# Optimization experiments

Measured on AMD Instinct MI355X. Metric: run time of the kernel, lower is better.

Reference implementation:

```python
import jax, jax.numpy as jnp
import numpy as np
from jax import lax

B, S, I, H, O, T = 8, 1024, 512, 1024, 512, 8
THRESH = 0.5


def setup_inputs() -> dict:
    key = jax.random.key(0)
    k = jax.random.split(key, 5)
    return {
        "x": jax.random.normal(k[0], (B, S, I), dtype=jnp.float32),
        "w1": jax.random.normal(k[1], (H, I), dtype=jnp.float32) * (1.0 / np.sqrt(I)),
        "b1": jax.random.normal(k[2], (H,), dtype=jnp.float32) * 0.01,
        "w2": jax.random.normal(k[3], (O, H), dtype=jnp.float32) * (1.0 / np.sqrt(H)),
        "b2": jax.random.normal(k[4], (O,), dtype=jnp.float32) * 0.01,
    }


def reference(x, w1, b1, w2, b2):
    # x: (B, S, I). Precompute the input current once (same every timestep).
    inp_cur = jnp.einsum("bsi,hi->bsh", x, w1) + b1  # (B, S, H)
    mem1_0 = jnp.zeros((B, S, H), dtype=x.dtype)
    mem2_0 = jnp.zeros((B, S, O), dtype=x.dtype)

    def step(carry, _):
        mem1, mem2 = carry
        mem1 = mem1 + inp_cur
        spike1 = (mem1 > THRESH).astype(x.dtype)
        mem1 = mem1 * (mem1 <= THRESH).astype(x.dtype)  # reset fired neurons
        mem2 = mem2 + jnp.einsum("bsh,oh->bso", spike1, w2) + b2
        spike2 = (mem2 > THRESH).astype(x.dtype)
        mem2 = mem2 * (mem2 <= THRESH).astype(x.dtype)
        return (mem1, mem2), spike2

    _, spikes = lax.scan(step, (mem1_0, mem2_0), None, length=T)  # (T, B, S, O)
    return jnp.moveaxis(spikes, 0, 1)  # stack on dim=1 -> (B, T, S, O)
```

## Files before the change

### kernel.cpp

```cpp
#include <hip/hip_runtime.h>

static constexpr int B_ = 8, S_ = 1024, I_ = 512, H_ = 1024, O_ = 512, T_ = 8;
static constexpr int M_ = B_ * S_;
static constexpr float TH = 0.5f;

__global__ __launch_bounds__(256) void k1(const float* __restrict__ X,
                                          const float* __restrict__ W1,
                                          const float* __restrict__ B1,
                                          unsigned char* __restrict__ SPB) {
  __shared__ float As[16][132];
  __shared__ float Bs[16][68];
  const int tid = threadIdx.x;
  const int tx = tid & 15, ty = tid >> 4;
  const int rowBase = blockIdx.x * 128, colBase = blockIdx.y * 64;
  const int rrA = tid >> 2, kqA = (tid & 3) << 2;
  const int rrB = tid >> 2, kqB = (tid & 3) << 2;

  float acc[8][4];
#pragma unroll
  for (int i = 0; i < 8; ++i)
#pragma unroll
    for (int j = 0; j < 4; ++j) acc[i][j] = 0.f;

  float4 pa0, pa1, pb;
#define K1_LOAD(IT)                                                            \
  {                                                                            \
    pa0 = *(const float4*)&X[(size_t)(rowBase + rrA) * I_ + (IT) * 16 + kqA];  \
    pa1 = *(const float4*)&X[(size_t)(rowBase + 64 + rrA) * I_ + (IT) * 16 + kqA]; \
    pb  = *(const float4*)&W1[(size_t)(colBase + rrB) * I_ + (IT) * 16 + kqB]; \
  }

  K1_LOAD(0);
  for (int it = 0; it < 32; ++it) {
    As[kqA + 0][rrA] = pa0.x; As[kqA + 1][rrA] = pa0.y;
    As[kqA + 2][rrA] = pa0.z; As[kqA + 3][rrA] = pa0.w;
    As[kqA + 0][64 + rrA] = pa1.x; As[kqA + 1][64 + rrA] = pa1.y;
    As[kqA + 2][64 + rrA] = pa1.z; As[kqA + 3][64 + rrA] = pa1.w;
    Bs[kqB + 0][rrB] = pb.x; Bs[kqB + 1][rrB] = pb.y;
    Bs[kqB + 2][rrB] = pb.z; Bs[kqB + 3][rrB] = pb.w;
    __syncthreads();
    if (it + 1 < 32) K1_LOAD(it + 1);
#pragma unroll
    for (int k = 0; k < 16; ++k) {
      float a[8], b[4];
      *(float4*)&a[0] = *(const float4*)&As[k][ty * 8];
      *(float4*)&a[4] = *(const float4*)&As[k][ty * 8 + 4];
      *(float4*)&b[0] = *(const float4*)&Bs[k][tx * 4];
#pragma unroll
      for (int i = 0; i < 8; ++i)
#pragma unroll
        for (int j = 0; j < 4; ++j) acc[i][j] = fmaf(a[i], b[j], acc[i][j]);
    }
    __syncthreads();
  }
#undef K1_LOAD

#pragma unroll
  for (int i = 0; i < 8; ++i) {
    int row = rowBase + ty * 8 + i;
    unsigned char by[4];
#pragma unroll
    for (int j = 0; j < 4; ++j) {
      int col = colBase + tx * 4 + j;
      float c = acc[i][j] + B1[col];
      float m = 0.f;
      unsigned bits = 0;
#pragma unroll
      for (int t = 0; t < 8; ++t) {
        m = m + c;
        bool s = m > TH;
        bits |= (s ? 1u : 0u) << t;
        m = s ? 0.f : m;
      }
      by[j] = (unsigned char)bits;
    }
    uchar4 pk; pk.x = by[0]; pk.y = by[1]; pk.z = by[2]; pk.w = by[3];
    *(uchar4*)&SPB[(size_t)row * H_ + colBase + tx * 4] = pk;
  }
}

__global__ __launch_bounds__(256) void k2(const unsigned char* __restrict__ SP,
                                          const float* __restrict__ W2,
                                          const float* __restrict__ B2,
                                          float* __restrict__ out, int t) {
  __shared__ float As0[16][68];
  __shared__ float As1[16][68];
  __shared__ float Bs0[16][68];
  __shared__ float Bs1[16][68];
  const int tid = threadIdx.x;
  const int tx = tid & 15, ty = tid >> 4;
  const int rowBase = blockIdx.x * 64, colBase = blockIdx.y * 64;
  const int rr = tid >> 2, bq = (tid & 3) << 2;

  float cur0[4][4], cur1[4][4];
#pragma unroll
  for (int i = 0; i < 4; ++i)
#pragma unroll
    for (int j = 0; j < 4; ++j) { cur0[i][j] = 0.f; cur1[i][j] = 0.f; }

  unsigned pu0, pu1;
  float4 pb0, pb1;
#define K2_LOAD(IT)                                                            \
  {                                                                            \
    const size_t rowOff = (size_t)(rowBase + rr) * H_;                         \
    pu0 = *(const unsigned*)&SP[rowOff + (IT) * 16 + bq];                      \
    pu1 = *(const unsigned*)&SP[rowOff + 512 + (IT) * 16 + bq];                \
    const size_t colOff = (size_t)(colBase + rr) * H_;                         \
    pb0 = *(const float4*)&W2[colOff + (IT) * 16 + bq];                        \
    pb1 = *(const float4*)&W2[colOff + 512 + (IT) * 16 + bq];                  \
  }

  K2_LOAD(0);
  for (int it = 0; it < 32; ++it) {
#pragma unroll
    for (int c = 0; c < 4; ++c) {
      As0[bq + c][rr] = (float)((pu0 >> (8 * c + t)) & 1u);
      As1[bq + c][rr] = (float)((pu1 >> (8 * c + t)) & 1u);
    }
    Bs0[bq + 0][rr] = pb0.x; Bs0[bq + 1][rr] = pb0.y;
    Bs0[bq + 2][rr] = pb0.z; Bs0[bq + 3][rr] = pb0.w;
    Bs1[bq + 0][rr] = pb1.x; Bs1[bq + 1][rr] = pb1.y;
    Bs1[bq + 2][rr] = pb1.z; Bs1[bq + 3][rr] = pb1.w;
    __syncthreads();
    if (it + 1 < 32) K2_LOAD(it + 1);
#pragma unroll
    for (int k = 0; k < 16; ++k) {
      float a0[4], b0[4], a1[4], b1v[4];
      *(float4*)&a0[0] = *(const float4*)&As0[k][ty * 4];
      *(float4*)&b0[0] = *(const float4*)&Bs0[k][tx * 4];
      *(float4*)&a1[0] = *(const float4*)&As1[k][ty * 4];
      *(float4*)&b1v[0] = *(const float4*)&Bs1[k][tx * 4];
#pragma unroll
      for (int i = 0; i < 4; ++i)
#pragma unroll
        for (int j = 0; j < 4; ++j) {
          cur0[i][j] = fmaf(a0[i], b0[j], cur0[i][j]);
          cur1[i][j] = fmaf(a1[i], b1v[j], cur1[i][j]);
        }
    }
    __syncthreads();
  }
#undef K2_LOAD

  const int col0 = colBase + tx * 4;
  float4 b2v = *(const float4*)&B2[col0];
#pragma unroll
  for (int i = 0; i < 4; ++i) {
    int row = rowBase + ty * 4 + i;
    int bb = row >> 10;
    int ss = row & (S_ - 1);
    size_t slot_t = (((size_t)bb * T_ + t) * S_ + ss) * O_ + col0;
    float4 mp;
    if (t == 0) mp = make_float4(0.f, 0.f, 0.f, 0.f);
    else mp = *(const float4*)&out[slot_t];
    float d[4], mm[4];
#pragma unroll
    for (int j = 0; j < 4; ++j)
      d[j] = cur0[i][j] + cur1[i][j];
    mm[0] = (mp.x + d[0]) + b2v.x;
    mm[1] = (mp.y + d[1]) + b2v.y;
    mm[2] = (mp.z + d[2]) + b2v.z;
    mm[3] = (mp.w + d[3]) + b2v.w;
    float4 sp, mn;
    sp.x = (mm[0] > TH) ? 1.f : 0.f;  mn.x = (mm[0] > TH) ? 0.f : mm[0];
    sp.y = (mm[1] > TH) ? 1.f : 0.f;  mn.y = (mm[1] > TH) ? 0.f : mm[1];
    sp.z = (mm[2] > TH) ? 1.f : 0.f;  mn.z = (mm[2] > TH) ? 0.f : mm[2];
    sp.w = (mm[3] > TH) ? 1.f : 0.f;  mn.w = (mm[3] > TH) ? 0.f : mm[3];
    *(float4*)&out[slot_t] = sp;
    if (t < T_ - 1) {
      size_t slot_n = (((size_t)bb * T_ + (t + 1)) * S_ + ss) * O_ + col0;
      *(float4*)&out[slot_n] = mn;
    }
  }
}

extern "C" void kernel_launch(void* const* d_in, const int* in_sizes, int n_in,
                              void* d_out, int out_size, void* d_ws, size_t ws_size,
                              hipStream_t stream) {
  const float* x  = (const float*)d_in[0];
  const float* w1 = (const float*)d_in[1];
  const float* b1 = (const float*)d_in[2];
  const float* w2 = (const float*)d_in[3];
  const float* b2 = (const float*)d_in[4];
  float* out = (float*)d_out;

  unsigned char* spikeB = (unsigned char*)d_ws;

  k1<<<dim3(M_ / 128, H_ / 64), 256, 0, stream>>>(x, w1, b1, spikeB);
  for (int t = 0; t < T_; ++t)
    k2<<<dim3(M_ / 64, O_ / 64), 256, 0, stream>>>(spikeB, w2, b2, out, t);
}
```

Measured before the change: 967.6 us.

## Batch four timesteps per GEMM launch, reusing W2 tiles across timesteps

Replaces the eight per-timestep spike×W2 GEMM launches with two launches, each handling four timesteps. Every row tile expands a row's spike byte into four timestep rows, so each W2 tile loaded into shared memory is reused across four timesteps. The membrane state is carried in registers within a launch and handed between launches through the t=4 output slot. Two partial sums over K halves keep the accumulation order close to the previous kernel. The cost is more accumulator registers per thread and a 32-row tile.

```diff
diff --git a/kernel.cpp b/kernel.cpp
--- a/kernel.cpp
+++ b/kernel.cpp
@@ -14,7 +14,6 @@
   const int tx = tid & 15, ty = tid >> 4;
   const int rowBase = blockIdx.x * 128, colBase = blockIdx.y * 64;
   const int rrA = tid >> 2, kqA = (tid & 3) << 2;
-  const int rrB = tid >> 2, kqB = (tid & 3) << 2;
 
   float acc[8][4];
 #pragma unroll
@@ -27,7 +26,7 @@
   {                                                                            \
     pa0 = *(const float4*)&X[(size_t)(rowBase + rrA) * I_ + (IT) * 16 + kqA];  \
     pa1 = *(const float4*)&X[(size_t)(rowBase + 64 + rrA) * I_ + (IT) * 16 + kqA]; \
-    pb  = *(const float4*)&W1[(size_t)(colBase + rrB) * I_ + (IT) * 16 + kqB]; \
+    pb  = *(const float4*)&W1[(size_t)(colBase + rrA) * I_ + (IT) * 16 + kqA]; \
   }
 
   K1_LOAD(0);
@@ -36,8 +35,8 @@
     As[kqA + 2][rrA] = pa0.z; As[kqA + 3][rrA] = pa0.w;
     As[kqA + 0][64 + rrA] = pa1.x; As[kqA + 1][64 + rrA] = pa1.y;
     As[kqA + 2][64 + rrA] = pa1.z; As[kqA + 3][64 + rrA] = pa1.w;
-    Bs[kqB + 0][rrB] = pb.x; Bs[kqB + 1][rrB] = pb.y;
-    Bs[kqB + 2][rrB] = pb.z; Bs[kqB + 3][rrB] = pb.w;
+    Bs[kqA + 0][rrA] = pb.x; Bs[kqA + 1][rrA] = pb.y;
+    Bs[kqA + 2][rrA] = pb.z; Bs[kqA + 3][rrA] = pb.w;
     __syncthreads();
     if (it + 1 < 32) K1_LOAD(it + 1);
 #pragma unroll
@@ -79,63 +78,73 @@
   }
 }
 
-__global__ __launch_bounds__(256) void k2(const unsigned char* __restrict__ SP,
-                                          const float* __restrict__ W2,
-                                          const float* __restrict__ B2,
-                                          float* __restrict__ out, int t) {
-  __shared__ float As0[16][68];
-  __shared__ float As1[16][68];
-  __shared__ float Bs0[16][68];
-  __shared__ float Bs1[16][68];
+__global__ __launch_bounds__(256) void k2f(const unsigned char* __restrict__ SP,
+                                           const float* __restrict__ W2,
+                                           const float* __restrict__ B2,
+                                           float* __restrict__ out, int tg) {
+  __shared__ float As[16][132];
+  __shared__ float Bs[16][68];
   const int tid = threadIdx.x;
   const int tx = tid & 15, ty = tid >> 4;
-  const int rowBase = blockIdx.x * 64, colBase = blockIdx.y * 64;
-  const int rr = tid >> 2, bq = (tid & 3) << 2;
-
-  float cur0[4][4], cur1[4][4];
-#pragma unroll
-  for (int i = 0; i < 4; ++i)
-#pragma unroll
-    for (int j = 0; j < 4; ++j) { cur0[i][j] = 0.f; cur1[i][j] = 0.f; }
-
-  unsigned pu0, pu1;
-  float4 pb0, pb1;
+  const int rowBase = blockIdx.x * 32, colBase = blockIdx.y * 64;
+  const int sr = tid >> 3;
+  const int sk = (tid & 7) << 1;
+  const int bc = tid >> 2;
+  const int bk = (tid & 3) << 2;
+  const int tb = tg * 4;
+
+  float tot[2][4][4], cur[2][4][4];
+#pragma unroll
+  for (int i = 0; i < 2; ++i)
+#pragma unroll
+    for (int j = 0; j < 4; ++j)
+#pragma unroll
+      for (int tt = 0; tt < 4; ++tt) { tot[i][j][tt] = 0.f; cur[i][j][tt] = 0.f; }
+
+  unsigned pu;
+  float4 pb;
 #define K2_LOAD(IT)                                                            \
   {                                                                            \
-    const size_t rowOff = (size_t)(rowBase + rr) * H_;                         \
-    pu0 = *(const unsigned*)&SP[rowOff + (IT) * 16 + bq];                      \
-    pu1 = *(const unsigned*)&SP[rowOff + 512 + (IT) * 16 + bq];                \
-    const size_t colOff = (size_t)(colBase + rr) * H_;                         \
-    pb0 = *(const float4*)&W2[colOff + (IT) * 16 + bq];                        \
-    pb1 = *(const float4*)&W2[colOff + 512 + (IT) * 16 + bq];                  \
+    pu = *(const unsigned short*)&SP[(size_t)(rowBase + sr) * H_ + (IT) * 16 + sk]; \
+    pb = *(const float4*)&W2[(size_t)(colBase + bc) * H_ + (IT) * 16 + bk];    \
   }
 
   K2_LOAD(0);
-  for (int it = 0; it < 32; ++it) {
-#pragma unroll
-    for (int c = 0; c < 4; ++c) {
-      As0[bq + c][rr] = (float)((pu0 >> (8 * c + t)) & 1u);
-      As1[bq + c][rr] = (float)((pu1 >> (8 * c + t)) & 1u);
-    }
-    Bs0[bq + 0][rr] = pb0.x; Bs0[bq + 1][rr] = pb0.y;
-    Bs0[bq + 2][rr] = pb0.z; Bs0[bq + 3][rr] = pb0.w;
-    Bs1[bq + 0][rr] = pb1.x; Bs1[bq + 1][rr] = pb1.y;
-    Bs1[bq + 2][rr] = pb1.z; Bs1[bq + 3][rr] = pb1.w;
-    __syncthreads();
-    if (it + 1 < 32) K2_LOAD(it + 1);
+  for (int it = 0; it < 64; ++it) {
+    if (it == 32) {
+#pragma unroll
+      for (int i = 0; i < 2; ++i)
+#pragma unroll
+        for (int j = 0; j < 4; ++j)
+#pragma unroll
+          for (int tt = 0; tt < 4; ++tt) {
+            tot[i][j][tt] += cur[i][j][tt];
+            cur[i][j][tt] = 0.f;
+          }
+    }
+    {
+      unsigned b0 = pu & 0xFFu, b1v = (pu >> 8) & 0xFFu;
+#pragma unroll
+      for (int tt = 0; tt < 4; ++tt) {
+        As[sk][sr * 4 + tt]     = (float)((b0 >> (tb + tt)) & 1u);
+        As[sk + 1][sr * 4 + tt] = (float)((b1v >> (tb + tt)) & 1u);
+      }
+      Bs[bk + 0][bc] = pb.x; Bs[bk + 1][bc] = pb.y;
+      Bs[bk + 2][bc] = pb.z; Bs[bk + 3][bc] = pb.w;
+    }
+    __syncthreads();
+    if (it + 1 < 64) K2_LOAD(it + 1);
 #pragma unroll
     for (int k = 0; k < 16; ++k) {
-      float a0[4], b0[4], a1[4], b1v[4];
-      *(float4*)&a0[0] = *(const float4*)&As0[k][ty * 4];
-      *(float4*)&b0[0] = *(const float4*)&Bs0[k][tx * 4];
-      *(float4*)&a1[0] = *(const float4*)&As1[k][ty * 4];
-      *(float4*)&b1v[0] = *(const float4*)&Bs1[k][tx * 4];
-#pragma unroll
-      for (int i = 0; i < 4; ++i)
-#pragma unroll
-        for (int j = 0; j < 4; ++j) {
-          cur0[i][j] = fmaf(a0[i], b0[j], cur0[i][j]);
-          cur1[i][j] = fmaf(a1[i], b1v[j], cur1[i][j]);
+      float4 a0 = *(const float4*)&As[k][(ty * 2) * 4];
+      float4 a1 = *(const float4*)&As[k][(ty * 2 + 1) * 4];
+      float4 b  = *(const float4*)&Bs[k][tx * 4];
+#pragma unroll
+      for (int j = 0; j < 4; ++j)
+#pragma unroll
+        for (int tt = 0; tt < 4; ++tt) {
+          cur[0][j][tt] = fmaf((&a0.x)[tt], (&b.x)[j], cur[0][j][tt]);
+          cur[1][j][tt] = fmaf((&a1.x)[tt], (&b.x)[j], cur[1][j][tt]);
         }
     }
     __syncthreads();
@@ -145,31 +154,36 @@
   const int col0 = colBase + tx * 4;
   float4 b2v = *(const float4*)&B2[col0];
 #pragma unroll
-  for (int i = 0; i < 4; ++i) {
-    int row = rowBase + ty * 4 + i;
+  for (int i = 0; i < 2; ++i) {
+    int row = rowBase + ty * 2 + i;
     int bb = row >> 10;
     int ss = row & (S_ - 1);
-    size_t slot_t = (((size_t)bb * T_ + t) * S_ + ss) * O_ + col0;
-    float4 mp;
-    if (t == 0) mp = make_float4(0.f, 0.f, 0.f, 0.f);
-    else mp = *(const float4*)&out[slot_t];
-    float d[4], mm[4];
-#pragma unroll
-    for (int j = 0; j < 4; ++j)
-      d[j] = cur0[i][j] + cur1[i][j];
-    mm[0] = (mp.x + d[0]) + b2v.x;
-    mm[1] = (mp.y + d[1]) + b2v.y;
-    mm[2] = (mp.z + d[2]) + b2v.z;
-    mm[3] = (mp.w + d[3]) + b2v.w;
-    float4 sp, mn;
-    sp.x = (mm[0] > TH) ? 1.f : 0.f;  mn.x = (mm[0] > TH) ? 0.f : mm[0];
-    sp.y = (mm[1] > TH) ? 1.f : 0.f;  mn.y = (mm[1] > TH) ? 0.f : mm[1];
-    sp.z = (mm[2] > TH) ? 1.f : 0.f;  mn.z = (mm[2] > TH) ? 0.f : mm[2];
-    sp.w = (mm[3] > TH) ? 1.f : 0.f;  mn.w = (mm[3] > TH) ? 0.f : mm[3];
-    *(float4*)&out[slot_t] = sp;
-    if (t < T_ - 1) {
-      size_t slot_n = (((size_t)bb * T_ + (t + 1)) * S_ + ss) * O_ + col0;
-      *(float4*)&out[slot_n] = mn;
+    size_t slot4 = (((size_t)bb * T_ + 4) * S_ + ss) * O_ + col0;
+    float mcur[4];
+    if (tg == 0) {
+      mcur[0] = 0.f; mcur[1] = 0.f; mcur[2] = 0.f; mcur[3] = 0.f;
+    } else {
+      float4 mp = *(const float4*)&out[slot4];
+      mcur[0] = mp.x; mcur[1] = mp.y; mcur[2] = mp.z; mcur[3] = mp.w;
+    }
+#pragma unroll
+    for (int tt = 0; tt < 4; ++tt) {
+      int t = tb + tt;
+      float4 sp;
+#pragma unroll
+      for (int j = 0; j < 4; ++j) {
+        float d = tot[i][j][tt] + cur[i][j][tt];
+        float v = (mcur[j] + d) + (&b2v.x)[j];
+        bool s = v > TH;
+        (&sp.x)[j] = s ? 1.f : 0.f;
+        mcur[j] = s ? 0.f : v;
+      }
+      *(float4*)&out[(((size_t)bb * T_ + t) * S_ + ss) * O_ + col0] = sp;
+    }
+    if (tg == 0) {
+      float4 mn;
+      mn.x = mcur[0]; mn.y = mcur[1]; mn.z = mcur[2]; mn.w = mcur[3];
+      *(float4*)&out[slot4] = mn;
     }
   }
 }
@@ -187,6 +201,6 @@
   unsigned char* spikeB = (unsigned char*)d_ws;
 
   k1<<<dim3(M_ / 128, H_ / 64), 256, 0, stream>>>(x, w1, b1, spikeB);
-  for (int t = 0; t < T_; ++t)
-    k2<<<dim3(M_ / 64, O_ / 64), 256, 0, stream>>>(spikeB, w2, b2, out, t);
+  k2f<<<dim3(M_ / 32, O_ / 64), 256, 0, stream>>>(spikeB, w2, b2, out, 0);
+  k2f<<<dim3(M_ / 32, O_ / 64), 256, 0, stream>>>(spikeB, w2, b2, out, 1);
 }
```

Result: faster. 842.5 us (-12.9%).
